# Performance work log

Hardware: AMD Instinct MI355X
Metric: run time of the kernel (lower is better)

The kernel has to match this reference:

```python
import jax, jax.numpy as jnp
import numpy as np

QUERY_SIZE = 512
KEY_SIZE = 512
VALUE_SIZE = 512
HIDDEN = 128


def setup_inputs() -> dict:
    key = jax.random.key(0)
    ks = jax.random.split(key, 9)
    b, t_q, t_k = 8, 128, 512
    query = jax.random.normal(ks[0], (b, t_q, QUERY_SIZE), dtype=jnp.float32)
    keys = jax.random.normal(ks[1], (b, t_k, KEY_SIZE), dtype=jnp.float32)
    values = jax.random.normal(ks[2], (b, t_k, VALUE_SIZE), dtype=jnp.float32)
    # torch nn.Linear init ~ U(-1/sqrt(fan_in), 1/sqrt(fan_in)); scale-matched normals are fine
    sq = 1.0 / np.sqrt(QUERY_SIZE)
    sk = 1.0 / np.sqrt(KEY_SIZE)
    sh = 1.0 / np.sqrt(HIDDEN)
    Wq = jax.random.uniform(ks[3], (HIDDEN, QUERY_SIZE), jnp.float32, -sq, sq)
    bq = jax.random.uniform(ks[4], (HIDDEN,), jnp.float32, -sq, sq)
    Wk = jax.random.uniform(ks[5], (HIDDEN, KEY_SIZE), jnp.float32, -sk, sk)
    bk = jax.random.uniform(ks[6], (HIDDEN,), jnp.float32, -sk, sk)
    Wo = jax.random.uniform(ks[7], (1, HIDDEN), jnp.float32, -sh, sh)
    bo = jax.random.uniform(ks[8], (1,), jnp.float32, -sh, sh)
    return {"query": query, "keys": keys, "values": values,
            "Wq": Wq, "bq": bq, "Wk": Wk, "bk": bk, "Wo": Wo, "bo": bo}


def reference(query, keys, values, Wq, bq, Wk, bk, Wo, bo):
    # Bahdanau additive attention: att_ij = Wo @ tanh(Wq q_i + Wk k_j + bq + bk) + bo
    # Project once per position (mathematically identical to the expanded per-pair Linear).
    q_proj = jnp.einsum('bqn,hn->bqh', query, Wq) + bq          # b x t_q x h
    k_proj = jnp.einsum('bkn,hn->bkh', keys, Wk) + bk           # b x t_k x h
    hid = jnp.tanh(q_proj[:, :, None, :] + k_proj[:, None, :, :])  # b x t_q x t_k x h
    scores = jnp.einsum('bqkh,h->bqk', hid, Wo[0]) + bo[0]       # b x t_q x t_k
    attn = jax.nn.softmax(scores, axis=2)
    context = jnp.einsum('bqk,bkv->bqv', attn, values)           # b x t_q x n_v
    return context, attn
```

## Files before the change

kernel.cpp:

```cpp
#include <hip/hip_runtime.h>


#define B_    8
#define TQ_   128
#define TK_   512
#define NIN_  512
#define H_    128
#define NV_   512
#define NQR   (B_*TQ_)
#define NROWS (NQR + B_*TK_)
#define CTXN  (B_*TQ_*NV_)

#define C2_   2.8853900817779268f
#define L2E_  1.4426950408889634f

__device__ __forceinline__ float fexp2(float x){ return __builtin_amdgcn_exp2f(x); }
__device__ __forceinline__ float frcp (float x){ return __builtin_amdgcn_rcpf(x); }

__global__ __launch_bounds__(256, 5) void proj_kernel(
        const float* __restrict__ query, const float* __restrict__ keys,
        const float* __restrict__ Wq, const float* __restrict__ Wk,
        float* __restrict__ psum, int kper) {
    __shared__ float at[32][18];
    __shared__ float wt[32][132];
    const int tid = threadIdx.x;
    const int r0  = blockIdx.x * 16;
    const float* in; const float* W;
    if (r0 < NQR) { in = query + (size_t)r0 * NIN_;         W = Wq; }
    else          { in = keys  + (size_t)(r0 - NQR) * NIN_; W = Wk; }

    const int r2 = (tid >> 5) * 2;
    const int h4 = (tid & 31) * 4;
    const int ar  = tid >> 4;
    const int ak2 = (tid & 15) * 2;
    const int wr  = tid >> 3;
    const int wkq = (tid & 7) * 4;
    const int kb0 = blockIdx.y * kper;
    const int nc  = kper >> 5;

    const float* pA  = in + (size_t)ar * NIN_ + kb0 + ak2;
    const float* pW0 = W + (size_t)(wr     ) * NIN_ + kb0 + wkq;
    const float* pW1 = W + (size_t)(wr + 32) * NIN_ + kb0 + wkq;
    const float* pW2 = W + (size_t)(wr + 64) * NIN_ + kb0 + wkq;
    const float* pW3 = W + (size_t)(wr + 96) * NIN_ + kb0 + wkq;

    float2 af = *(const float2*)pA;
    float4 w0 = *(const float4*)pW0, w1 = *(const float4*)pW1;
    float4 w2 = *(const float4*)pW2, w3 = *(const float4*)pW3;

    float acc[2][4] = {{0.f,0.f,0.f,0.f},{0.f,0.f,0.f,0.f}};

    for (int c = 0; c < nc; ++c) {
        __syncthreads();
        at[ak2+0][ar] = af.x; at[ak2+1][ar] = af.y;
        wt[wkq+0][wr   ] = w0.x; wt[wkq+1][wr   ] = w0.y;
        wt[wkq+2][wr   ] = w0.z; wt[wkq+3][wr   ] = w0.w;
        wt[wkq+0][wr+32] = w1.x; wt[wkq+1][wr+32] = w1.y;
        wt[wkq+2][wr+32] = w1.z; wt[wkq+3][wr+32] = w1.w;
        wt[wkq+0][wr+64] = w2.x; wt[wkq+1][wr+64] = w2.y;
        wt[wkq+2][wr+64] = w2.z; wt[wkq+3][wr+64] = w2.w;
        wt[wkq+0][wr+96] = w3.x; wt[wkq+1][wr+96] = w3.y;
        wt[wkq+2][wr+96] = w3.z; wt[wkq+3][wr+96] = w3.w;
        __syncthreads();
        if (c + 1 < nc) {
            pA += 32; pW0 += 32; pW1 += 32; pW2 += 32; pW3 += 32;
            af = *(const float2*)pA;
            w0 = *(const float4*)pW0; w1 = *(const float4*)pW1;
            w2 = *(const float4*)pW2; w3 = *(const float4*)pW3;
        }
#pragma unroll 8
        for (int kk = 0; kk < 32; ++kk) {
            const float2 a = *(const float2*)&at[kk][r2];
            const float4 w = *(const float4*)&wt[kk][h4];
            acc[0][0] = fmaf(a.x, w.x, acc[0][0]);
            acc[0][1] = fmaf(a.x, w.y, acc[0][1]);
            acc[0][2] = fmaf(a.x, w.z, acc[0][2]);
            acc[0][3] = fmaf(a.x, w.w, acc[0][3]);
            acc[1][0] = fmaf(a.y, w.x, acc[1][0]);
            acc[1][1] = fmaf(a.y, w.y, acc[1][1]);
            acc[1][2] = fmaf(a.y, w.z, acc[1][2]);
            acc[1][3] = fmaf(a.y, w.w, acc[1][3]);
        }
    }

    float* op = psum + ((size_t)blockIdx.y * NROWS + r0) * H_;
#pragma unroll
    for (int i = 0; i < 2; ++i) {
        float4 o = {acc[i][0], acc[i][1], acc[i][2], acc[i][3]};
        *(float4*)&op[(size_t)(r2 + i) * H_ + h4] = o;
    }
}

__global__ __launch_bounds__(256, 4) void reduceP_kernel(
        const float* __restrict__ psum, const float* __restrict__ bq,
        const float* __restrict__ bk, float* __restrict__ pout) {
    const int tid = threadIdx.x;
    const int r0  = blockIdx.x * 8;
    const float* bias = (r0 < NQR) ? bq : bk;
    const int row = tid >> 5, hq = (tid & 31) * 4;
    float4 s = *(const float4*)&bias[hq];
#pragma unroll
    for (int sp = 0; sp < 4; ++sp) {
        float4 v = *(const float4*)&psum[((size_t)sp * NROWS + r0 + row) * H_ + hq];
        s.x += v.x; s.y += v.y; s.z += v.z; s.w += v.w;
    }
    float4 o = {s.x * C2_, s.y * C2_, s.z * C2_, s.w * C2_};
    *(float4*)&pout[(size_t)(r0 + row) * H_ + hq] = o;
}

__global__ __launch_bounds__(256, 4) void scores_kernel(
        const float* __restrict__ qp, const float* __restrict__ kp,
        const float* __restrict__ Wo, const float* __restrict__ bo,
        float* __restrict__ out_attn) {
    __shared__ float qs2[2][H_];
    __shared__ float w2[H_];
    __shared__ float sc[2][TK_];

    const int tid = threadIdx.x;
    const int b   = blockIdx.y;
    const int q0  = blockIdx.x * 2;
    const int lane = tid & 63;

    qs2[tid >> 7][tid & 127] =
        qp[(size_t)(b * TQ_ + q0 + (tid >> 7)) * H_ + (tid & 127)];
    if (tid < H_) w2[tid] = Wo[tid] * -2.0f;
    __syncthreads();

    float sw = w2[lane] + w2[lane + 64];
#pragma unroll
    for (int m = 1; m < 64; m <<= 1) sw += __shfl_xor(sw, m);
    const float sbase = bo[0] - 0.5f * sw;

#pragma unroll
    for (int half = 0; half < 2; ++half) {
        const int k = tid + half * 256;
        const float4* kp4 = (const float4*)&kp[(size_t)(b * TK_ + k) * H_];
        float s0 = 0.f, s1 = 0.f;
#pragma unroll 4
        for (int hb = 0; hb < 32; ++hb) {
            const float4 kv  = kp4[hb];
            const float4 wv  = *(const float4*)&w2[hb * 4];
            const float4 q0v = *(const float4*)&qs2[0][hb * 4];
            const float4 q1v = *(const float4*)&qs2[1][hb * 4];
            s0 = fmaf(wv.x, frcp(fexp2(q0v.x + kv.x) + 1.f), s0);
            s0 = fmaf(wv.y, frcp(fexp2(q0v.y + kv.y) + 1.f), s0);
            s0 = fmaf(wv.z, frcp(fexp2(q0v.z + kv.z) + 1.f), s0);
            s0 = fmaf(wv.w, frcp(fexp2(q0v.w + kv.w) + 1.f), s0);
            s1 = fmaf(wv.x, frcp(fexp2(q1v.x + kv.x) + 1.f), s1);
            s1 = fmaf(wv.y, frcp(fexp2(q1v.y + kv.y) + 1.f), s1);
            s1 = fmaf(wv.z, frcp(fexp2(q1v.z + kv.z) + 1.f), s1);
            s1 = fmaf(wv.w, frcp(fexp2(q1v.w + kv.w) + 1.f), s1);
        }
        sc[0][k] = s0 + sbase;
        sc[1][k] = s1 + sbase;
    }
    __syncthreads();

    const int w = tid >> 6;
    if (w < 2) {
        float4 sA = *(const float4*)&sc[w][lane * 8];
        float4 sB = *(const float4*)&sc[w][lane * 8 + 4];
        float m = fmaxf(fmaxf(fmaxf(sA.x, sA.y), fmaxf(sA.z, sA.w)),
                        fmaxf(fmaxf(sB.x, sB.y), fmaxf(sB.z, sB.w)));
#pragma unroll
        for (int mk = 1; mk < 64; mk <<= 1) m = fmaxf(m, __shfl_xor(m, mk));
        float4 eA, eB;
        eA.x = fexp2((sA.x - m) * L2E_); eA.y = fexp2((sA.y - m) * L2E_);
        eA.z = fexp2((sA.z - m) * L2E_); eA.w = fexp2((sA.w - m) * L2E_);
        eB.x = fexp2((sB.x - m) * L2E_); eB.y = fexp2((sB.y - m) * L2E_);
        eB.z = fexp2((sB.z - m) * L2E_); eB.w = fexp2((sB.w - m) * L2E_);
        float s = eA.x + eA.y + eA.z + eA.w + eB.x + eB.y + eB.z + eB.w;
#pragma unroll
        for (int mk = 1; mk < 64; mk <<= 1) s += __shfl_xor(s, mk);
        const float inv = frcp(s);
        eA.x *= inv; eA.y *= inv; eA.z *= inv; eA.w *= inv;
        eB.x *= inv; eB.y *= inv; eB.z *= inv; eB.w *= inv;
        float4* op = (float4*)&out_attn[(size_t)(b * TQ_ + q0 + w) * TK_ + lane * 8];
        op[0] = eA; op[1] = eB;
    }
}

__global__ __launch_bounds__(128, 4) void context_kernel(
        const float* __restrict__ attn, const float* __restrict__ values,
        float* __restrict__ psumC) {
    __shared__ float at[32][18];
    __shared__ float vt[32][68];

    const int tid = threadIdx.x;
    const int r0  = blockIdx.x * 16;
    const int b   = r0 >> 7;
    const int v0  = blockIdx.y * 64;
    const int kb0 = blockIdx.z * 128;

    const int q2 = (tid >> 4) * 2;
    const int v4 = (tid & 15) * 4;
    const int ar  = tid >> 3;
    const int akq = (tid & 7) * 4;
    const int vr  = tid >> 4;
    const int vq  = (tid & 15) * 4;

    const float* pAt = attn + (size_t)(r0 + ar) * TK_ + kb0 + akq;
    const float* pV0 = values + (size_t)(b * TK_ + kb0 + vr     ) * NV_ + v0 + vq;
    const float* pV1 = values + (size_t)(b * TK_ + kb0 + vr +  8) * NV_ + v0 + vq;
    const float* pV2 = values + (size_t)(b * TK_ + kb0 + vr + 16) * NV_ + v0 + vq;
    const float* pV3 = values + (size_t)(b * TK_ + kb0 + vr + 24) * NV_ + v0 + vq;

    float4 af  = *(const float4*)pAt;
    float4 vf0 = *(const float4*)pV0;
    float4 vf1 = *(const float4*)pV1;
    float4 vf2 = *(const float4*)pV2;
    float4 vf3 = *(const float4*)pV3;

    float acc[2][4] = {{0.f,0.f,0.f,0.f},{0.f,0.f,0.f,0.f}};

    for (int c = 0; c < 4; ++c) {
        __syncthreads();
        at[akq+0][ar] = af.x; at[akq+1][ar] = af.y;
        at[akq+2][ar] = af.z; at[akq+3][ar] = af.w;
        *(float4*)&vt[vr     ][vq] = vf0;
        *(float4*)&vt[vr +  8][vq] = vf1;
        *(float4*)&vt[vr + 16][vq] = vf2;
        *(float4*)&vt[vr + 24][vq] = vf3;
        __syncthreads();
        if (c + 1 < 4) {
            pAt += 32; pV0 += 32 * NV_; pV1 += 32 * NV_;
            pV2 += 32 * NV_; pV3 += 32 * NV_;
            af  = *(const float4*)pAt;
            vf0 = *(const float4*)pV0; vf1 = *(const float4*)pV1;
            vf2 = *(const float4*)pV2; vf3 = *(const float4*)pV3;
        }
#pragma unroll 8
        for (int kk = 0; kk < 32; ++kk) {
            const float2 a = *(const float2*)&at[kk][q2];
            const float4 v = *(const float4*)&vt[kk][v4];
            acc[0][0] = fmaf(a.x, v.x, acc[0][0]);
            acc[0][1] = fmaf(a.x, v.y, acc[0][1]);
            acc[0][2] = fmaf(a.x, v.z, acc[0][2]);
            acc[0][3] = fmaf(a.x, v.w, acc[0][3]);
            acc[1][0] = fmaf(a.y, v.x, acc[1][0]);
            acc[1][1] = fmaf(a.y, v.y, acc[1][1]);
            acc[1][2] = fmaf(a.y, v.z, acc[1][2]);
            acc[1][3] = fmaf(a.y, v.w, acc[1][3]);
        }
    }

    float* op = psumC + (size_t)blockIdx.z * CTXN + (size_t)r0 * NV_ + v0;
#pragma unroll
    for (int i = 0; i < 2; ++i) {
        float4 o = {acc[i][0], acc[i][1], acc[i][2], acc[i][3]};
        *(float4*)&op[(size_t)(q2 + i) * NV_ + v4] = o;
    }
}

__global__ __launch_bounds__(256, 4) void reduceC_kernel(
        const float* __restrict__ psumC, float* __restrict__ outc) {
    const size_t i = ((size_t)blockIdx.x * 256 + threadIdx.x) * 4;
    float4 s = *(const float4*)&psumC[i];
#pragma unroll
    for (int z = 1; z < 4; ++z) {
        float4 v = *(const float4*)&psumC[(size_t)z * CTXN + i];
        s.x += v.x; s.y += v.y; s.z += v.z; s.w += v.w;
    }
    *(float4*)&outc[i] = s;
}

extern "C" void kernel_launch(void* const* d_in, const int* in_sizes, int n_in,
                              void* d_out, int out_size, void* d_ws, size_t ws_size,
                              hipStream_t stream) {
    const float* query  = (const float*)d_in[0];
    const float* keys   = (const float*)d_in[1];
    const float* values = (const float*)d_in[2];
    const float* Wq     = (const float*)d_in[3];
    const float* bq     = (const float*)d_in[4];
    const float* Wk     = (const float*)d_in[5];
    const float* bk     = (const float*)d_in[6];
    const float* Wo     = (const float*)d_in[7];
    const float* bo     = (const float*)d_in[8];

    float* out_ctx  = (float*)d_out;
    float* out_attn = out_ctx + B_ * TQ_ * NV_;
    float* pout  = (float*)d_ws;
    float* qp    = pout;
    float* kp    = pout + (size_t)NQR * H_;
    float* psumP = pout + (size_t)NROWS * H_;
    float* psumC = psumP + (size_t)4 * NROWS * H_;

    proj_kernel<<<dim3(NROWS / 16, 4), 256, 0, stream>>>(
        query, keys, Wq, Wk, psumP, NIN_ / 4);
    reduceP_kernel<<<NROWS / 8, 256, 0, stream>>>(psumP, bq, bk, pout);
    scores_kernel<<<dim3(TQ_ / 2, B_), 256, 0, stream>>>(qp, kp, Wo, bo, out_attn);
    context_kernel<<<dim3(NQR / 16, NV_ / 64, 4), 128, 0, stream>>>(
        out_attn, values, psumC);
    reduceC_kernel<<<CTXN / 1024, 256, 0, stream>>>(psumC, out_ctx);
}
```

Before: 66.10 us.

## Replace split-K context GEMM and reduction with single-pass full-K context kernel

The context kernel no longer splits the key dimension four ways into partial sums followed by a separate reduction kernel. Each 256-thread block now stages 8 attention rows in shared memory and walks all 512 keys, reading values directly from global memory and writing the final output. This removes the psumC round-trip through global memory and one kernel launch. In exchange, each value element is reused across only 8 queries per block, values are read straight from global memory without LDS tiling, and the grid shrinks to 512 blocks, so more global/L2 traffic on values and less latency hiding are possible.

Measured after the change: 78.38 us. 1.19x slower.

```diff
diff --git a/kernel.cpp b/kernel.cpp
--- a/kernel.cpp
+++ b/kernel.cpp
@@ -9,7 +9,6 @@
 #define NV_   512
 #define NQR   (B_*TQ_)
 #define NROWS (NQR + B_*TK_)
-#define CTXN  (B_*TQ_*NV_)
 
 #define C2_   2.8853900817779268f
 #define L2E_  1.4426950408889634f
@@ -180,88 +179,41 @@
     }
 }
 
-__global__ __launch_bounds__(128, 4) void context_kernel(
+__global__ __launch_bounds__(256, 2) void context_kernel(
         const float* __restrict__ attn, const float* __restrict__ values,
-        float* __restrict__ psumC) {
-    __shared__ float at[32][18];
-    __shared__ float vt[32][68];
-
-    const int tid = threadIdx.x;
-    const int r0  = blockIdx.x * 16;
-    const int b   = r0 >> 7;
-    const int v0  = blockIdx.y * 64;
-    const int kb0 = blockIdx.z * 128;
-
-    const int q2 = (tid >> 4) * 2;
-    const int v4 = (tid & 15) * 4;
-    const int ar  = tid >> 3;
-    const int akq = (tid & 7) * 4;
-    const int vr  = tid >> 4;
-    const int vq  = (tid & 15) * 4;
-
-    const float* pAt = attn + (size_t)(r0 + ar) * TK_ + kb0 + akq;
-    const float* pV0 = values + (size_t)(b * TK_ + kb0 + vr     ) * NV_ + v0 + vq;
-    const float* pV1 = values + (size_t)(b * TK_ + kb0 + vr +  8) * NV_ + v0 + vq;
-    const float* pV2 = values + (size_t)(b * TK_ + kb0 + vr + 16) * NV_ + v0 + vq;
-    const float* pV3 = values + (size_t)(b * TK_ + kb0 + vr + 24) * NV_ + v0 + vq;
-
-    float4 af  = *(const float4*)pAt;
-    float4 vf0 = *(const float4*)pV0;
-    float4 vf1 = *(const float4*)pV1;
-    float4 vf2 = *(const float4*)pV2;
-    float4 vf3 = *(const float4*)pV3;
-
-    float acc[2][4] = {{0.f,0.f,0.f,0.f},{0.f,0.f,0.f,0.f}};
-
-    for (int c = 0; c < 4; ++c) {
-        __syncthreads();
-        at[akq+0][ar] = af.x; at[akq+1][ar] = af.y;
-        at[akq+2][ar] = af.z; at[akq+3][ar] = af.w;
-        *(float4*)&vt[vr     ][vq] = vf0;
-        *(float4*)&vt[vr +  8][vq] = vf1;
-        *(float4*)&vt[vr + 16][vq] = vf2;
-        *(float4*)&vt[vr + 24][vq] = vf3;
-        __syncthreads();
-        if (c + 1 < 4) {
-            pAt += 32; pV0 += 32 * NV_; pV1 += 32 * NV_;
-            pV2 += 32 * NV_; pV3 += 32 * NV_;
-            af  = *(const float4*)pAt;
-            vf0 = *(const float4*)pV0; vf1 = *(const float4*)pV1;
-            vf2 = *(const float4*)pV2; vf3 = *(const float4*)pV3;
-        }
+        float* __restrict__ outc) {
+    __shared__ float asm_[8][TK_];
+
+    const int tid  = threadIdx.x;
+    const int pair = blockIdx.x & 31;
+    const int qt   = blockIdx.x >> 5;
+    const int b    = pair >> 2;
+    const int v0   = (pair & 3) * 128;
+    const int q0   = qt * 8;
+
+#pragma unroll
+    for (int p = 0; p < 4; ++p) {
+        const int idx = tid + p * 256;
+        const int row = idx >> 7, kq = (idx & 127) * 4;
+        *(float4*)&asm_[row][kq] =
+            *(const float4*)&attn[(size_t)(b * TQ_ + q0 + row) * TK_ + kq];
+    }
+    __syncthreads();
+
+    const int q  = tid >> 5;
+    const int v4 = v0 + (tid & 31) * 4;
+    const float* vp = values + (size_t)b * TK_ * NV_ + v4;
+    float4 acc = {0.f, 0.f, 0.f, 0.f};
 #pragma unroll 8
-        for (int kk = 0; kk < 32; ++kk) {
-            const float2 a = *(const float2*)&at[kk][q2];
-            const float4 v = *(const float4*)&vt[kk][v4];
-            acc[0][0] = fmaf(a.x, v.x, acc[0][0]);
-            acc[0][1] = fmaf(a.x, v.y, acc[0][1]);
-            acc[0][2] = fmaf(a.x, v.z, acc[0][2]);
-            acc[0][3] = fmaf(a.x, v.w, acc[0][3]);
-            acc[1][0] = fmaf(a.y, v.x, acc[1][0]);
-            acc[1][1] = fmaf(a.y, v.y, acc[1][1]);
-            acc[1][2] = fmaf(a.y, v.z, acc[1][2]);
-            acc[1][3] = fmaf(a.y, v.w, acc[1][3]);
-        }
-    }
-
-    float* op = psumC + (size_t)blockIdx.z * CTXN + (size_t)r0 * NV_ + v0;
-#pragma unroll
-    for (int i = 0; i < 2; ++i) {
-        float4 o = {acc[i][0], acc[i][1], acc[i][2], acc[i][3]};
-        *(float4*)&op[(size_t)(q2 + i) * NV_ + v4] = o;
-    }
-}
-
-__global__ __launch_bounds__(256, 4) void reduceC_kernel(
-        const float* __restrict__ psumC, float* __restrict__ outc) {
-    const size_t i = ((size_t)blockIdx.x * 256 + threadIdx.x) * 4;
-    float4 s = *(const float4*)&psumC[i];
-#pragma unroll
-    for (int z = 1; z < 4; ++z) {
-        float4 v = *(const float4*)&psumC[(size_t)z * CTXN + i];
-        s.x += v.x; s.y += v.y; s.z += v.z; s.w += v.w;
-    }
-    *(float4*)&outc[i] = s;
+    for (int k = 0; k < TK_; ++k) {
+        const float4 vv = *(const float4*)&vp[(size_t)k * NV_];
+        const float a = asm_[q][k];
+        acc.x = fmaf(a, vv.x, acc.x);
+        acc.y = fmaf(a, vv.y, acc.y);
+        acc.z = fmaf(a, vv.z, acc.z);
+        acc.w = fmaf(a, vv.w, acc.w);
+    }
+    *(float4*)&outc[(size_t)(b * TQ_ + q0 + q) * NV_ + v4] = acc;
 }
 
 extern "C" void kernel_launch(void* const* d_in, const int* in_sizes, int n_in,
@@ -283,13 +235,10 @@
     float* qp    = pout;
     float* kp    = pout + (size_t)NQR * H_;
     float* psumP = pout + (size_t)NROWS * H_;
-    float* psumC = psumP + (size_t)4 * NROWS * H_;
 
     proj_kernel<<<dim3(NROWS / 16, 4), 256, 0, stream>>>(
         query, keys, Wq, Wk, psumP, NIN_ / 4);
     reduceP_kernel<<<NROWS / 8, 256, 0, stream>>>(psumP, bq, bk, pout);
     scores_kernel<<<dim3(TQ_ / 2, B_), 256, 0, stream>>>(qp, kp, Wo, bo, out_attn);
-    context_kernel<<<dim3(NQR / 16, NV_ / 64, 4), 128, 0, stream>>>(
-        out_attn, values, psumC);
-    reduceC_kernel<<<CTXN / 1024, 256, 0, stream>>>(psumC, out_ctx);
-}
+    context_kernel<<<512, 256, 0, stream>>>(out_attn, values, out_ctx);
+}
```
